# Optimization experiments

Hardware: AMD Instinct MI355X
Metric: run time of the kernel (lower is better)

## Reference

```python
import jax, jax.numpy as jnp
import numpy as np

N_HEADS = 16


def _rope_tables(seq_len, head_dim, dtype):
    # matches torch RoPE.__init__: inv_freq over head_dim, outer with positions
    inv_freq = 1.0 / (10000.0 ** (jnp.arange(0, head_dim, 2, dtype=jnp.float32) / head_dim))
    t = jnp.arange(seq_len, dtype=jnp.float32)
    freqs = jnp.outer(t, inv_freq)  # [T, head_dim//2]
    return jnp.cos(freqs).astype(dtype), jnp.sin(freqs).astype(dtype)


def _apply_rope(x, cos, sin):
    # x: [B, H, T, Dh]; interleaved even/odd rotation
    x_even = x[..., ::2]
    x_odd = x[..., 1::2]
    rot_even = x_even * cos - x_odd * sin
    rot_odd = x_even * sin + x_odd * cos
    return jnp.stack([rot_even, rot_odd], axis=-1).reshape(x.shape)


def setup_inputs() -> dict:
    key = jax.random.key(0)
    ks = jax.random.split(key, 5)
    B, T, D = 4, 1024, 1024
    s = 1.0 / np.sqrt(D)
    return {
        "x": jax.random.normal(ks[0], (B, T, D), dtype=jnp.float32),
        "Wq": jax.random.normal(ks[1], (D, D), dtype=jnp.float32) * s,
        "Wk": jax.random.normal(ks[2], (D, D), dtype=jnp.float32) * s,
        "Wv": jax.random.normal(ks[3], (D, D), dtype=jnp.float32) * s,
        "Wo": jax.random.normal(ks[4], (D, D), dtype=jnp.float32) * s,
    }


def reference(x, Wq, Wk, Wv, Wo):
    B, T, D = x.shape
    H = N_HEADS
    Dh = D // H

    def proj(W):
        # nn.Linear: x @ W.T ; reshape to [B, H, T, Dh]
        return (x @ W.T).reshape(B, T, H, Dh).transpose(0, 2, 1, 3)

    q, k, v = proj(Wq), proj(Wk), proj(Wv)
    cos, sin = _rope_tables(T, Dh, x.dtype)
    q = _apply_rope(q, cos, sin)
    k = _apply_rope(k, cos, sin)

    # NOTE: original module applies NO 1/sqrt(Dh) scaling
    scores = jnp.einsum("bhqd,bhkd->bhqk", q, k)
    causal = jnp.tril(jnp.ones((T, T), dtype=bool))
    scores = jnp.where(causal, scores, -jnp.inf)
    attn = jax.nn.softmax(scores, axis=-1)
    out = jnp.einsum("bhqk,bhkd->bhqd", attn, v)
    out = out.transpose(0, 2, 1, 3).reshape(B, T, D)
    return out @ Wo.T
```

## Files before the change

### kernel.cpp

```cpp
#include <hip/hip_runtime.h>
#include <stdint.h>

typedef unsigned short u16;
typedef short s16x8 __attribute__((ext_vector_type(8)));
typedef __bf16 bf16x8 __attribute__((ext_vector_type(8)));
typedef _Float16 f16x8 __attribute__((ext_vector_type(8)));
typedef float f32x4 __attribute__((ext_vector_type(4)));

#define SEQ    1024
#define DMODEL 1024
#define NB     4
#define NH     16
#define DH     64
#define QBLK   128
#define KVB    64
#define LOG2E  1.4426950408889634f

__device__ __forceinline__ u16 f2bf(float f) {
  uint32_t u = __builtin_bit_cast(uint32_t, f);
  u += 0x7fffu + ((u >> 16) & 1u);
  return (u16)(u >> 16);
}
__device__ __forceinline__ u16 f2bf_rz(float f) {
  return (u16)(__builtin_bit_cast(uint32_t, f) >> 16);
}
__device__ __forceinline__ float bf2f(u16 h) {
  uint32_t u = ((uint32_t)h) << 16;
  return __builtin_bit_cast(float, u);
}
__device__ __forceinline__ u16 f2h(float f) {
  return __builtin_bit_cast(u16, (_Float16)f);
}
__device__ __forceinline__ float h2f(u16 u) {
  return (float)__builtin_bit_cast(_Float16, u);
}

#define MFMA16(a, b, c)  __builtin_amdgcn_mfma_f32_16x16x32_bf16((a), (b), (c), 0, 0, 0)
#define MFMA16H(a, b, c) __builtin_amdgcn_mfma_f32_16x16x32_f16((a), (b), (c), 0, 0, 0)

template<bool F16>
__device__ __forceinline__ f32x4 MF(s16x8 a, s16x8 b, f32x4 c) {
  if constexpr (F16)
    return MFMA16H(__builtin_bit_cast(f16x8, a), __builtin_bit_cast(f16x8, b), c);
  else
    return MFMA16(__builtin_bit_cast(bf16x8, a), __builtin_bit_cast(bf16x8, b), c);
}

__device__ __forceinline__ void gload_lds16(const u16* g, uintptr_t lds_addr) {
  __builtin_amdgcn_global_load_lds(
      (__attribute__((address_space(1))) void*)(uintptr_t)g,
      (__attribute__((address_space(3))) void*)lds_addr,
      16, 0, 0);
}

__global__ void cast_all_kernel(
    const float* __restrict__ x, const float* __restrict__ wq,
    const float* __restrict__ wk, const float* __restrict__ wv,
    const float* __restrict__ wo,
    u16* __restrict__ xd, u16* __restrict__ wqd, u16* __restrict__ wkd,
    u16* __restrict__ wvd, u16* __restrict__ wod)
{
  const int NX = (NB * SEQ * DMODEL) / 8;
  const int NW = (DMODEL * DMODEL) / 8;
  int c = blockIdx.x * blockDim.x + threadIdx.x;
  const float* src; u16* dst; bool tobf = false;
  if (c < NX)                { src = x;  dst = xd; }
  else if ((c -= NX) < NW)   { src = wq; dst = wqd; }
  else if ((c -= NW) < NW)   { src = wk; dst = wkd; }
  else if ((c -= NW) < NW)   { src = wv; dst = wvd; }
  else if ((c -= NW) < NW)   { src = wo; dst = wod; tobf = true; }
  else return;
  float f[8];
  float4 v0 = *(const float4*)(src + (size_t)c * 8);
  float4 v1 = *(const float4*)(src + (size_t)c * 8 + 4);
  f[0] = v0.x; f[1] = v0.y; f[2] = v0.z; f[3] = v0.w;
  f[4] = v1.x; f[5] = v1.y; f[6] = v1.z; f[7] = v1.w;
  union { u16 u[8]; uint4 v; } H;
#pragma unroll
  for (int e = 0; e < 8; ++e) H.u[e] = tobf ? f2bf(f[e]) : f2h(f[e]);
  *(uint4*)(dst + (size_t)c * 8) = H.v;
}

__global__ void rope_kernel(u16* __restrict__ Q, u16* __restrict__ K) {
  const int nP = (NB * SEQ) * (DMODEL / 2);
  int idx = blockIdx.x * blockDim.x + threadIdx.x;
  u16* buf; int p;
  if (idx < nP) { buf = Q; p = idx; }
  else          { buf = K; p = idx - nP; }
  int row = p >> 9;
  int pi  = p & 511;
  int t   = row & (SEQ - 1);
  int fi  = pi & 31;
  float inv = exp2f((float)fi * (-13.287712379549449f / 32.0f));
  float ang = (float)t * inv;
  float sn, cs;
  sincosf(ang, &sn, &cs);
  size_t off = (size_t)row * DMODEL + pi * 2;
  uint32_t v = *(uint32_t*)(buf + off);
  float e = h2f((u16)(v & 0xffffu));
  float o = h2f((u16)(v >> 16));
  float re = e * cs - o * sn;
  float ro = e * sn + o * cs;
  *(uint32_t*)(buf + off) = (uint32_t)f2h(re) | ((uint32_t)f2h(ro) << 16);
}

struct GemmPtrs {
  const u16* B[3]; u16* C0[3]; int mode[3];
};

template<bool F16, int BN>
__global__ __launch_bounds__(256) void gemm_bt_kernel(
    const u16* __restrict__ A,
    GemmPtrs P, float* __restrict__ CF,
    int M, int N, int K, int out_f32)
{
  constexpr int NF = BN / 32;
  constexpr int BCH = BN / 32;
  __shared__ __align__(16) u16 sA[128 * 64];
  __shared__ __align__(16) u16 sB[BN * 64];
  const int t = threadIdx.x, lane = t & 63;
  const int wave = t >> 6;
  const int g = lane >> 4, cl = lane & 15;
  const int z = blockIdx.z;
  const u16* B = P.B[z];
  const int n0 = blockIdx.x * BN, m0 = blockIdx.y * 128;
  const int wr = wave >> 1, wc = wave & 1;

  int srow[4], scol[4], soff[4];
#pragma unroll
  for (int j = 0; j < 4; ++j) {
    int c = j * 256 + t;
    srow[j] = c >> 3;
    scol[j] = ((c & 7) ^ (srow[j] & 7)) * 8;
    soff[j] = c * 16;
  }

  f32x4 acc[4][NF] = {};

  for (int k0 = 0; k0 < K; k0 += 64) {
#pragma unroll
    for (int j = 0; j < 4; ++j)
      gload_lds16(A + (size_t)(m0 + srow[j]) * K + k0 + scol[j], (uintptr_t)sA + soff[j]);
#pragma unroll
    for (int j = 0; j < BCH; ++j)
      gload_lds16(B + (size_t)(n0 + srow[j]) * K + k0 + scol[j], (uintptr_t)sB + soff[j]);
    __syncthreads();

    s16x8 af[4][2];
#pragma unroll
    for (int m = 0; m < 4; ++m) {
      int row = wr * 64 + m * 16 + cl;
#pragma unroll
      for (int kk = 0; kk < 2; ++kk)
        af[m][kk] = *(const s16x8*)&sA[row * 64 + (((kk * 4 + g) ^ (row & 7)) * 8)];
    }
#pragma unroll
    for (int n = 0; n < NF; ++n) {
      int row = wc * (BN / 2) + n * 16 + cl;
      s16x8 b0 = *(const s16x8*)&sB[row * 64 + ((g ^ (row & 7)) * 8)];
      s16x8 b1 = *(const s16x8*)&sB[row * 64 + (((4 + g) ^ (row & 7)) * 8)];
#pragma unroll
      for (int m = 0; m < 4; ++m) {
        acc[m][n] = MF<F16>(af[m][0], b0, acc[m][n]);
        acc[m][n] = MF<F16>(af[m][1], b1, acc[m][n]);
      }
    }
    __syncthreads();
  }

  if (out_f32) {
#pragma unroll
    for (int m = 0; m < 4; ++m)
#pragma unroll
      for (int n = 0; n < NF; ++n)
#pragma unroll
        for (int r = 0; r < 4; ++r) {
          int row = m0 + wr * 64 + m * 16 + g * 4 + r;
          int col = n0 + wc * (BN / 2) + n * 16 + cl;
          CF[(size_t)row * N + col] = acc[m][n][r];
        }
  } else if (P.mode[z] == 1) {
    u16* VT = P.C0[z];
#pragma unroll
    for (int m = 0; m < 4; ++m)
#pragma unroll
      for (int n = 0; n < NF; ++n) {
        int row0 = m0 + wr * 64 + m * 16 + g * 4;
        int col = n0 + wc * (BN / 2) + n * 16 + cl;
        union { u16 u[4]; uint2 v; } pk;
#pragma unroll
        for (int r = 0; r < 4; ++r) pk.u[r] = f2bf(acc[m][n][r]);
        *(uint2*)&VT[(size_t)col * M + row0] = pk.v;
      }
  } else {
    u16* C = P.C0[z];
#pragma unroll
    for (int m = 0; m < 4; ++m)
#pragma unroll
      for (int n = 0; n < NF; ++n)
#pragma unroll
        for (int r = 0; r < 4; ++r) {
          int row = m0 + wr * 64 + m * 16 + g * 4 + r;
          int col = n0 + wc * (BN / 2) + n * 16 + cl;
          float v = acc[m][n][r];
          C[(size_t)row * N + col] = F16 ? f2h(v) : f2bf(v);
        }
  }
}

__global__ __launch_bounds__(256, 2) void attn_kernel(
    const u16* __restrict__ Q, const u16* __restrict__ K,
    const u16* __restrict__ Vt,
    u16* __restrict__ Oh)
{
  __shared__ __align__(16) u16 sK [2][KVB * 64];
  __shared__ __align__(16) u16 sVt[2][DH * KVB];
  __shared__ __align__(16) u16 sP[128 * 72];

  const int t = threadIdx.x, lane = t & 63, wave = t >> 6;
  const int g = lane >> 4, cl = lane & 15;
  const int h = blockIdx.x & (NH - 1), b = blockIdx.x >> 4;
  const int y = blockIdx.y;
  const int qi = (y < 4) ? (7 - y) : (y - 4);
  const int q0 = qi * QBLK;
  const size_t rowbase = (size_t)b * SEQ;
  const int colbase = h * DH;
  const int MT = NB * SEQ;

  const u16* Kb  = K + rowbase * DMODEL + colbase;
  const u16* Vtb = Vt + (size_t)(h * DH) * MT + b * SEQ;

  int srow[2], scol[2], soff[2];
#pragma unroll
  for (int j = 0; j < 2; ++j) {
    int c = j * 256 + t;
    srow[j] = c >> 3;
    scol[j] = ((c & 7) ^ (srow[j] & 7)) * 8;
    soff[j] = c * 16;
  }

  int koff0[4], koff1[4];
#pragma unroll
  for (int n = 0; n < 4; ++n) {
    int row = n * 16 + cl;
    koff0[n] = row * 64 + ((g ^ (row & 7)) * 8);
    koff1[n] = row * 64 + (((4 + g) ^ (row & 7)) * 8);
  }
  int paoff[2][2];
#pragma unroll
  for (int kk = 0; kk < 2; ++kk) {
    paoff[kk][0] = (wave * 32 + cl) * 72 + kk * 32 + g * 8;
    paoff[kk][1] = (wave * 32 + 16 + cl) * 72 + kk * 32 + g * 8;
  }

  f16x8 qf[2][2];
#pragma unroll
  for (int mf = 0; mf < 2; ++mf) {
    int qrow = q0 + wave * 32 + mf * 16 + cl;
    const u16* pq = Q + (rowbase + qrow) * DMODEL + colbase + g * 8;
    qf[mf][0] = __builtin_bit_cast(f16x8, *(const s16x8*)pq);
    qf[mf][1] = __builtin_bit_cast(f16x8, *(const s16x8*)(pq + 32));
  }

  bf16x8 ones;
#pragma unroll
  for (int e = 0; e < 8; ++e) ones[e] = (__bf16)1.0f;

  f32x4 o_acc[2][4] = {};
  f32x4 o_l[2] = {};

  const int last = 2 * qi + 1;
  const int wrow0 = q0 + wave * 32;
  const int prow0 = wave * 32;

#pragma unroll
  for (int j = 0; j < 2; ++j) {
    gload_lds16(Kb + (size_t)srow[j] * DMODEL + scol[j],  (uintptr_t)&sK[0][0] + soff[j]);
    gload_lds16(Vtb + (size_t)srow[j] * MT + scol[j],     (uintptr_t)&sVt[0][0] + soff[j]);
  }
  __syncthreads();

  int cur = 0;
  for (int kt = 0; kt <= last; ++kt) {
    const int kv0 = kt * KVB;
    if (kt < last) {
      const int nk = kv0 + KVB;
#pragma unroll
      for (int j = 0; j < 2; ++j) {
        gload_lds16(Kb + (size_t)(nk + srow[j]) * DMODEL + scol[j],
                    (uintptr_t)&sK[cur ^ 1][0] + soff[j]);
        gload_lds16(Vtb + (size_t)srow[j] * MT + nk + scol[j],
                    (uintptr_t)&sVt[cur ^ 1][0] + soff[j]);
      }
    }

    const bool skip = (wrow0 + 31) < kv0;
    if (!skip) {
      const bool needmask = (kv0 + 63) > wrow0;

      f32x4 s[2][4];
      __builtin_amdgcn_s_setprio(1);
#pragma unroll
      for (int n = 0; n < 4; ++n) {
        f16x8 k0 = __builtin_bit_cast(f16x8, *(const s16x8*)&sK[cur][koff0[n]]);
        f16x8 k1 = __builtin_bit_cast(f16x8, *(const s16x8*)&sK[cur][koff1[n]]);
#pragma unroll
        for (int mf = 0; mf < 2; ++mf) {
          f32x4 zz = {};
          zz = MFMA16H(qf[mf][0], k0, zz);
          zz = MFMA16H(qf[mf][1], k1, zz);
          s[mf][n] = zz;
        }
      }
      __builtin_amdgcn_s_setprio(0);

#pragma unroll
      for (int mf = 0; mf < 2; ++mf) {
#pragma unroll
        for (int r = 0; r < 4; ++r) {
          int qg = wrow0 + mf * 16 + g * 4 + r;
          int prow = prow0 + mf * 16 + g * 4 + r;
#pragma unroll
          for (int n = 0; n < 4; ++n) {
            float p = exp2f(s[mf][n][r] * LOG2E);
            if (needmask && (kv0 + n * 16 + cl > qg)) p = 0.0f;
            sP[prow * 72 + n * 16 + cl] = f2bf_rz(p);
          }
        }
      }

      __builtin_amdgcn_s_setprio(1);
#pragma unroll
      for (int kk = 0; kk < 2; ++kk) {
        bf16x8 pa0 = *(const bf16x8*)&sP[paoff[kk][0]];
        bf16x8 pa1 = *(const bf16x8*)&sP[paoff[kk][1]];
#pragma unroll
        for (int n = 0; n < 4; ++n) {
          bf16x8 vf = *(const bf16x8*)&sVt[cur][(kk == 0) ? koff0[n] : koff1[n]];
          o_acc[0][n] = MFMA16(pa0, vf, o_acc[0][n]);
          o_acc[1][n] = MFMA16(pa1, vf, o_acc[1][n]);
        }
        o_l[0] = MFMA16(pa0, ones, o_l[0]);
        o_l[1] = MFMA16(pa1, ones, o_l[1]);
      }
      __builtin_amdgcn_s_setprio(0);
    }

    __syncthreads();
    cur ^= 1;
  }

#pragma unroll
  for (int mf = 0; mf < 2; ++mf)
#pragma unroll
    for (int n = 0; n < 4; ++n)
#pragma unroll
      for (int r = 0; r < 4; ++r) {
        float ov = o_acc[mf][n][r] / o_l[mf][r];
        int qrow = q0 + wave * 32 + mf * 16 + g * 4 + r;
        size_t idx = (rowbase + qrow) * DMODEL + colbase + n * 16 + cl;
        Oh[idx] = f2bf(ov);
      }
}

extern "C" void kernel_launch(void* const* d_in, const int* in_sizes, int n_in,
                              void* d_out, int out_size, void* d_ws, size_t ws_size,
                              hipStream_t stream) {
  const float* x  = (const float*)d_in[0];
  const float* Wq = (const float*)d_in[1];
  const float* Wk = (const float*)d_in[2];
  const float* Wv = (const float*)d_in[3];
  const float* Wo = (const float*)d_in[4];
  float* out = (float*)d_out;

  const int M = NB * SEQ;
  const int D = DMODEL;
  char* ws = (char*)d_ws;
  const size_t MB = 1u << 20;
  u16* xh16 = (u16*)(ws + 0 * MB);
  u16* qh16 = (u16*)(ws + 8 * MB);
  u16* kh16 = (u16*)(ws + 16 * MB);
  u16* vt   = (u16*)(ws + 24 * MB);
  u16* oh   = (u16*)(ws + 40 * MB);
  u16* wq16 = (u16*)(ws + 48 * MB);
  u16* wk16 = (u16*)(ws + 50 * MB);
  u16* wv16 = (u16*)(ws + 52 * MB);
  u16* wob  = (u16*)(ws + 54 * MB);

  {
    int total = M * D / 8 + 4 * (D * D / 8);
    cast_all_kernel<<<(total + 255) / 256, 256, 0, stream>>>(
        x, Wq, Wk, Wv, Wo, xh16, wq16, wk16, wv16, wob);
  }

  {
    GemmPtrs P;
    P.B[0] = wq16; P.B[1] = wk16; P.B[2] = wv16;
    P.C0[0] = qh16; P.C0[1] = kh16; P.C0[2] = vt;
    P.mode[0] = 0; P.mode[1] = 0; P.mode[2] = 1;
    gemm_bt_kernel<true, 128><<<dim3(D / 128, M / 128, 3), 256, 0, stream>>>(
        xh16, P, nullptr, M, D, D, 0);
  }

  rope_kernel<<<(2 * M * (D / 2) + 255) / 256, 256, 0, stream>>>(qh16, kh16);

  attn_kernel<<<dim3(NH * NB, 8), 256, 0, stream>>>(qh16, kh16, vt, oh);

  {
    GemmPtrs P;
    P.B[0] = wob; P.B[1] = wob; P.B[2] = wob;
    P.C0[0] = nullptr; P.C0[1] = nullptr; P.C0[2] = nullptr;
    P.mode[0] = 0; P.mode[1] = 0; P.mode[2] = 0;
    gemm_bt_kernel<false, 64><<<dim3(D / 64, M / 128, 1), 256, 0, stream>>>(
        oh, P, out, M, D, D, 1);
  }
}
```

Measured before the change: 104.7 us.

## Fuse RoPE into QK projection GEMM epilogue with precomputed cos/sin table

Removes the standalone RoPE pass over Q and K and applies the rotation inside the projection GEMM's epilogue. Each lane gets its even/odd partner value through a lane shuffle. A small kernel precomputes a per-position cos/sin table, which the epilogue loads into reused shared memory. This avoids an extra read-modify-write of Q and K in global memory and a kernel launch. In exchange the GEMM epilogue gains a shared-memory table load, a barrier and a shuffle, and rotation is now done in fp32 before the fp16 rounding.

```diff
diff --git a/kernel.cpp b/kernel.cpp
--- a/kernel.cpp
+++ b/kernel.cpp
@@ -51,6 +51,16 @@
       (__attribute__((address_space(1))) void*)(uintptr_t)g,
       (__attribute__((address_space(3))) void*)lds_addr,
       16, 0, 0);
+}
+
+__global__ void rope_table_kernel(float2* __restrict__ tab) {
+  int i = blockIdx.x * blockDim.x + threadIdx.x;
+  int t = i >> 5, fi = i & 31;
+  float inv = exp2f((float)fi * (-13.287712379549449f / 32.0f));
+  float ang = (float)t * inv;
+  float sn, cs;
+  sincosf(ang, &sn, &cs);
+  tab[i] = make_float2(cs, sn);
 }
 
 __global__ void cast_all_kernel(
@@ -81,43 +91,21 @@
   *(uint4*)(dst + (size_t)c * 8) = H.v;
 }
 
-__global__ void rope_kernel(u16* __restrict__ Q, u16* __restrict__ K) {
-  const int nP = (NB * SEQ) * (DMODEL / 2);
-  int idx = blockIdx.x * blockDim.x + threadIdx.x;
-  u16* buf; int p;
-  if (idx < nP) { buf = Q; p = idx; }
-  else          { buf = K; p = idx - nP; }
-  int row = p >> 9;
-  int pi  = p & 511;
-  int t   = row & (SEQ - 1);
-  int fi  = pi & 31;
-  float inv = exp2f((float)fi * (-13.287712379549449f / 32.0f));
-  float ang = (float)t * inv;
-  float sn, cs;
-  sincosf(ang, &sn, &cs);
-  size_t off = (size_t)row * DMODEL + pi * 2;
-  uint32_t v = *(uint32_t*)(buf + off);
-  float e = h2f((u16)(v & 0xffffu));
-  float o = h2f((u16)(v >> 16));
-  float re = e * cs - o * sn;
-  float ro = e * sn + o * cs;
-  *(uint32_t*)(buf + off) = (uint32_t)f2h(re) | ((uint32_t)f2h(ro) << 16);
-}
-
 struct GemmPtrs {
-  const u16* B[3]; u16* C0[3]; int mode[3];
+  const u16* B[3]; u16* C0[3]; int mode[3]; int rope[3];
 };
 
 template<bool F16, int BN>
 __global__ __launch_bounds__(256) void gemm_bt_kernel(
     const u16* __restrict__ A,
-    GemmPtrs P, float* __restrict__ CF,
+    GemmPtrs P, float* __restrict__ CF, const float2* __restrict__ ropetab,
     int M, int N, int K, int out_f32)
 {
   constexpr int NF = BN / 32;
   constexpr int BCH = BN / 32;
-  __shared__ __align__(16) u16 sA[128 * 64];
-  __shared__ __align__(16) u16 sB[BN * 64];
+  __shared__ __align__(16) u16 smem[128 * 64 + BN * 64];
+  u16* sA = smem;
+  u16* sB = smem + 128 * 64;
   const int t = threadIdx.x, lane = t & 63;
   const int wave = t >> 6;
   const int g = lane >> 4, cl = lane & 15;
@@ -194,6 +182,18 @@
       }
   } else {
     u16* C = P.C0[z];
+    const bool dorope = (BN == 128) && (P.rope[z] != 0);
+    float2* sTab = (float2*)smem;
+    if (dorope) {
+      const u16* tsrc = (const u16*)(ropetab + (size_t)(m0 & (SEQ - 1)) * 32);
+#pragma unroll
+      for (int j = 0; j < 8; ++j) {
+        int c = j * 256 + t;
+        gload_lds16(tsrc + c * 8, (uintptr_t)sTab + c * 16);
+      }
+      __syncthreads();
+    }
+    const bool oddl = lane & 1;
 #pragma unroll
     for (int m = 0; m < 4; ++m)
 #pragma unroll
@@ -203,6 +203,12 @@
           int row = m0 + wr * 64 + m * 16 + g * 4 + r;
           int col = n0 + wc * (BN / 2) + n * 16 + cl;
           float v = acc[m][n][r];
+          if (dorope) {
+            float2 cs = sTab[(row - m0) * 32 + ((n * 16 + cl) >> 1)];
+            float pv = __shfl_xor(v, 1);
+            v = oddl ? (pv * cs.y + v * cs.x)
+                     : (v * cs.x - pv * cs.y);
+          }
           C[(size_t)row * N + col] = F16 ? f2h(v) : f2bf(v);
         }
   }
@@ -386,7 +392,9 @@
   u16* wk16 = (u16*)(ws + 50 * MB);
   u16* wv16 = (u16*)(ws + 52 * MB);
   u16* wob  = (u16*)(ws + 54 * MB);
-
+  float2* ropetab = (float2*)(ws + 56 * MB);
+
+  rope_table_kernel<<<SEQ * 32 / 256, 256, 0, stream>>>(ropetab);
   {
     int total = M * D / 8 + 4 * (D * D / 8);
     cast_all_kernel<<<(total + 255) / 256, 256, 0, stream>>>(
@@ -398,11 +406,10 @@
     P.B[0] = wq16; P.B[1] = wk16; P.B[2] = wv16;
     P.C0[0] = qh16; P.C0[1] = kh16; P.C0[2] = vt;
     P.mode[0] = 0; P.mode[1] = 0; P.mode[2] = 1;
+    P.rope[0] = 1; P.rope[1] = 1; P.rope[2] = 0;
     gemm_bt_kernel<true, 128><<<dim3(D / 128, M / 128, 3), 256, 0, stream>>>(
-        xh16, P, nullptr, M, D, D, 0);
-  }
-
-  rope_kernel<<<(2 * M * (D / 2) + 255) / 256, 256, 0, stream>>>(qh16, kh16);
+        xh16, P, nullptr, ropetab, M, D, D, 0);
+  }
 
   attn_kernel<<<dim3(NH * NB, 8), 256, 0, stream>>>(qh16, kh16, vt, oh);
 
@@ -411,7 +418,8 @@
     P.B[0] = wob; P.B[1] = wob; P.B[2] = wob;
     P.C0[0] = nullptr; P.C0[1] = nullptr; P.C0[2] = nullptr;
     P.mode[0] = 0; P.mode[1] = 0; P.mode[2] = 0;
+    P.rope[0] = 0; P.rope[1] = 0; P.rope[2] = 0;
     gemm_bt_kernel<false, 64><<<dim3(D / 64, M / 128, 1), 256, 0, stream>>>(
-        oh, P, out, M, D, D, 1);
-  }
-}
+        oh, P, out, nullptr, M, D, D, 1);
+  }
+}
```

New measurement: 119.0 us. 1.14x slower.
